# Kernel optimization log

Measured on AMD Instinct MI355X. Metric: run time of the kernel, lower is better.

Reference implementation:

```python
import jax, jax.numpy as jnp
import numpy as np

B, F_IN, C_NODES, M = 8, 32, 256, 64
C_OUT = 64
ORDER = 2
N_BASES = 3


def setup_inputs() -> dict:
    key = jax.random.key(0)
    ks = jax.random.split(key, 6)
    x = jax.random.normal(ks[0], (B, F_IN, C_NODES, M), dtype=jnp.float32)
    base0 = jax.random.uniform(ks[1], (B, M, C_NODES, C_NODES), dtype=jnp.float32) / C_NODES
    base1 = jax.random.uniform(ks[2], (B, M, C_NODES, C_NODES), dtype=jnp.float32) / C_NODES
    base2 = jax.random.uniform(ks[3], (B, M, C_NODES, C_NODES), dtype=jnp.float32) / C_NODES
    c_cat = (ORDER * N_BASES + 1) * F_IN  # 224
    W = jax.random.normal(ks[4], (C_OUT, c_cat), dtype=jnp.float32) * (1.0 / np.sqrt(c_cat))
    b = jnp.zeros((C_OUT,), dtype=jnp.float32)
    return {"x": x, "base0": base0, "base1": base1, "base2": base2, "W": W, "b": b}


def _nconv(x, A):
    # x: [B, F, n, M], A: [B, M, n, v] -> [B, F, v, M]
    return jnp.einsum('bfnm,bmnv->bfvm', x, A)


def reference(x, base0, base1, base2, W, b):
    out = [x]
    for A in (base0, base1, base2):
        x1 = _nconv(x, A)
        out.append(x1)
        for _ in range(2, ORDER + 1):
            x1 = _nconv(x1, A)
            out.append(x1)
    h = jnp.concatenate(out, axis=1)  # [B, 7F, C, M]
    # 1x1 conv == channel-mixing GEMM
    y = jnp.einsum('of,bfcm->bocm', W, h) + b[None, :, None, None]
    return y
```

## Files before the change

kernel.cpp:

```cpp
#include <hip/hip_runtime.h>

typedef __attribute__((ext_vector_type(8))) short short8;
typedef __attribute__((ext_vector_type(4))) float floatx4;
typedef unsigned short u16;
typedef unsigned int u32;

#define MFMA16(a,b,c) __builtin_amdgcn_mfma_f32_16x16x32_bf16((a),(b),(c),0,0,0)

#define GLD_LDS16(src, dst)                                                    \
  __builtin_amdgcn_global_load_lds(                                            \
      (const __attribute__((address_space(1))) u32*)(const u32*)(src),         \
      (__attribute__((address_space(3))) u32*)(u32*)(dst), 16, 0, 0)

#define WAITVM(N)                                                              \
  do {                                                                         \
    asm volatile("s_waitcnt vmcnt(" #N ")" ::: "memory");                      \
    __builtin_amdgcn_sched_barrier(0);                                         \
  } while (0)

#define WAITLGKM0() asm volatile("s_waitcnt lgkmcnt(0)" ::: "memory")

__device__ __forceinline__ void bar_lds() {
  WAITLGKM0();
  __builtin_amdgcn_s_barrier();
  asm volatile("" ::: "memory");
}

__device__ __forceinline__ u16 f2bf(float f) {
  u32 u = __builtin_bit_cast(u32, f);
  u += 0x7fffu + ((u >> 16) & 1u);
  return (u16)(u >> 16);
}
__device__ __forceinline__ u32 pk2(float a, float b) {
  return (u32)f2bf(a) | ((u32)f2bf(b) << 16);
}

__global__ __launch_bounds__(256) void tk_f2b(const float* __restrict__ in,
                                              u16* __restrict__ out,
                                              int NI, int NJ) {
  __shared__ float tile[64][65];
  const int tid = threadIdx.x;
  const long long base = (long long)blockIdx.z * NI * NJ;
  const int i0 = blockIdx.x * 64, j0 = blockIdx.y * 64;
#pragma unroll
  for (int p = 0; p < 4; ++p) {
    int i = p * 16 + (tid >> 4);
    int jl = (tid & 15) * 4;
    float4 v = *(const float4*)(in + base + (long long)(i0 + i) * NJ + j0 + jl);
    tile[i][jl + 0] = v.x; tile[i][jl + 1] = v.y;
    tile[i][jl + 2] = v.z; tile[i][jl + 3] = v.w;
  }
  __syncthreads();
#pragma unroll
  for (int p = 0; p < 4; ++p) {
    int j = p * 16 + (tid >> 4);
    int il = (tid & 15) * 4;
    float e0 = tile[il + 0][j], e1 = tile[il + 1][j];
    float e2 = tile[il + 2][j], e3 = tile[il + 3][j];
    uint2 o; o.x = pk2(e0, e1); o.y = pk2(e2, e3);
    *(uint2*)(out + base + (long long)(j0 + j) * NI + i0 + il) = o;
  }
}

__global__ __launch_bounds__(256) void tk_f2f(const float* __restrict__ in,
                                              float* __restrict__ out,
                                              int NI, int NJ) {
  __shared__ float tile[64][65];
  const int tid = threadIdx.x;
  const long long base = (long long)blockIdx.z * NI * NJ;
  const int i0 = blockIdx.x * 64, j0 = blockIdx.y * 64;
#pragma unroll
  for (int p = 0; p < 4; ++p) {
    int i = p * 16 + (tid >> 4);
    int jl = (tid & 15) * 4;
    float4 v = *(const float4*)(in + base + (long long)(i0 + i) * NJ + j0 + jl);
    tile[i][jl + 0] = v.x; tile[i][jl + 1] = v.y;
    tile[i][jl + 2] = v.z; tile[i][jl + 3] = v.w;
  }
  __syncthreads();
#pragma unroll
  for (int p = 0; p < 4; ++p) {
    int j = p * 16 + (tid >> 4);
    int il = (tid & 15) * 4;
    float4 o;
    o.x = tile[il + 0][j]; o.y = tile[il + 1][j];
    o.z = tile[il + 2][j]; o.w = tile[il + 3][j];
    *(float4*)(out + base + (long long)(j0 + j) * NI + i0 + il) = o;
  }
}

__global__ __launch_bounds__(256, 2) void gcn_main(
    const u16* __restrict__ xT, const float* __restrict__ A0,
    const float* __restrict__ A1, const float* __restrict__ A2,
    const float* __restrict__ Wm, const float* __restrict__ bias,
    float* __restrict__ yT) {
  __shared__ __align__(16) unsigned char smem[81920];
  unsigned char* ring   = smem;
  unsigned char* fragX1 = smem + 49152;
  unsigned char* fragH  = smem + 65536;

  const int tid  = threadIdx.x;
  const int w    = tid >> 6;
  const int lane = tid & 63;
  const int q    = lane >> 4;
  const int s    = lane & 15;
  const int wg   = blockIdx.x;

  const float* Acur  = A0 + (size_t)wg * 65536;
  const float* Anxt  = A1 + (size_t)wg * 65536;
  const float* Alast = A2 + (size_t)wg * 65536;

  const int lrow = (lane >> 4) << 8;
  const int lc0  = (w << 6) + ((lane & 15) << 2);
  const int lc1  = lc0 ^ 16;
  char* wring = (char*)ring + (w << 12);

  auto stage = [&](const float* Ap, int c, int slot) {
#pragma unroll
    for (int i = 0; i < 4; ++i) {
      const float* src = Ap + (c << 12) + (i << 10) + lrow + ((i & 2) ? lc1 : lc0);
      GLD_LDS16(src, wring + slot * 16384 + (i << 10));
    }
  };

  stage(Acur, 0, 0);
  stage(Acur, 1, 1);
  stage(Acur, 2, 2);

  short8 xa[2][8];
  const u16* xp = xT + (size_t)wg * 8192;
#pragma unroll
  for (int mr = 0; mr < 2; ++mr)
#pragma unroll
    for (int k = 0; k < 8; ++k)
      xa[mr][k] = *(const short8*)(xp + (16 * mr + s) * 256 + 32 * k + 8 * q);

#pragma unroll
  for (int mr = 0; mr < 2; ++mr)
#pragma unroll
    for (int kk = 0; kk < 8; ++kk) {
      if ((kk >> 1) != w) continue;
#pragma unroll
      for (int jj = 0; jj < 8; ++jj) {
        int c = 32 * kk + 8 * q + jj;
        int f = 16 * mr + s;
        int off = (((c >> 4) * 64 + (f >> 3) * 16 + (c & 15)) << 4) + 2 * (f & 7);
        *(u16*)(fragH + off) = (u16)xa[mr][kk][jj];
      }
    }

  floatx4 yacc[4][4];
#pragma unroll
  for (int mr = 0; mr < 4; ++mr)
#pragma unroll
    for (int t = 0; t < 4; ++t) yacc[mr][t] = (floatx4){0.f, 0.f, 0.f, 0.f};

  auto finalGemm = [&](int jblk) {
    short8 wf[4], hf[4];
#pragma unroll
    for (int mr = 0; mr < 4; ++mr) {
      const float* wp = Wm + (16 * mr + s) * 224 + 32 * jblk + 8 * q;
      float4 lo = *(const float4*)wp;
      float4 hi = *(const float4*)(wp + 4);
      union { uint4 u; short8 v; } r;
      r.u.x = pk2(lo.x, lo.y); r.u.y = pk2(lo.z, lo.w);
      r.u.z = pk2(hi.x, hi.y); r.u.w = pk2(hi.z, hi.w);
      wf[mr] = r.v;
    }
#pragma unroll
    for (int t = 0; t < 4; ++t)
      hf[t] = *(const short8*)(fragH + (((4 * w + t) * 64 + lane) << 4));
#pragma unroll
    for (int mr = 0; mr < 4; ++mr)
#pragma unroll
      for (int t = 0; t < 4; ++t)
        yacc[mr][t] = MFMA16(wf[mr], hf[t], yacc[mr][t]);
  };
  auto writeH = [&](const floatx4 (&acc)[2][4]) {
#pragma unroll
    for (int mr = 0; mr < 2; ++mr)
#pragma unroll
      for (int t = 0; t < 4; ++t)
#pragma unroll
        for (int r = 0; r < 4; ++r) {
          int F = 16 * mr + 4 * q + r;
          int off = (((4 * w + t) * 64 + (F >> 3) * 16 + s) << 4) + 2 * (F & 7);
          *(u16*)(fragH + off) = f2bf(acc[mr][t][r]);
        }
  };
  auto writeX1 = [&](const floatx4 (&acc)[2][4]) {
#pragma unroll
    for (int mr = 0; mr < 2; ++mr)
#pragma unroll
      for (int t = 0; t < 4; ++t) {
        int Cc = 64 * w + 16 * t + s;
        int kk = Cc >> 5, qq = (Cc >> 3) & 3, jj = Cc & 7;
#pragma unroll
        for (int r = 0; r < 4; ++r) {
          int off = (((mr * 8 + kk) * 64 + qq * 16 + 4 * q + r) << 4) + 2 * jj;
          *(u16*)(fragX1 + off) = f2bf(acc[mr][t][r]);
        }
      }
  };

  auto fetchB = [&](int sl0, int sl1, short8 (&bf)[4]) {
    const char* bse = (const char*)ring + ((q >= 2) ? sl1 : sl0) * 16384 +
                      (w << 12) + ((q & 1) << 11);
    const int pvx = (q & 1) << 4;
#pragma unroll
    for (int t = 0; t < 4; ++t) {
      const float* fp = (const float*)(bse + ((((t << 4) + s) ^ pvx) << 2));
      union { uint4 u; short8 v; } r;
      r.u.x = pk2(fp[0],   fp[64]);
      r.u.y = pk2(fp[128], fp[192]);
      r.u.z = pk2(fp[256], fp[320]);
      r.u.w = pk2(fp[384], fp[448]);
      bf[t] = r.v;
    }
  };

  finalGemm(0);

#pragma unroll 1
  for (int ib = 0; ib < 3; ++ib) {
    floatx4 h1[2][4];
#pragma unroll
    for (int mr = 0; mr < 2; ++mr)
#pragma unroll
      for (int t = 0; t < 4; ++t) h1[mr][t] = (floatx4){0.f, 0.f, 0.f, 0.f};
#pragma unroll
    for (int kk = 0; kk < 8; ++kk) {
      if (kk < 7) WAITVM(4); else WAITVM(0);
      short8 bf[4];
      fetchB((2 * kk) % 3, (2 * kk + 1) % 3, bf);
#pragma unroll
      for (int mr = 0; mr < 2; ++mr)
#pragma unroll
        for (int t = 0; t < 4; ++t)
          h1[mr][t] = MFMA16(xa[mr][kk], bf[t], h1[mr][t]);
      WAITLGKM0();
      if (kk < 6) {
        stage(Acur, 2 * kk + 3, (2 * kk + 3) % 3);
        stage(Acur, 2 * kk + 4, (2 * kk + 4) % 3);
      } else if (kk == 6) {
        stage(Acur, 15, 0);
      } else {
        stage(Acur, 0, 0); stage(Acur, 1, 1); stage(Acur, 2, 2);
      }
    }
    bar_lds();
    writeX1(h1);
    writeH(h1);
    bar_lds();
    finalGemm(1 + 2 * ib);

    floatx4 h2[2][4];
#pragma unroll
    for (int mr = 0; mr < 2; ++mr)
#pragma unroll
      for (int t = 0; t < 4; ++t) h2[mr][t] = (floatx4){0.f, 0.f, 0.f, 0.f};
#pragma unroll
    for (int kk = 0; kk < 8; ++kk) {
      if (kk < 7) WAITVM(4); else WAITVM(0);
      short8 bf[4];
      fetchB((2 * kk) % 3, (2 * kk + 1) % 3, bf);
      short8 a0 = *(const short8*)(fragX1 + ((kk * 64 + lane) << 4));
      short8 a1 = *(const short8*)(fragX1 + (((8 + kk) * 64 + lane) << 4));
#pragma unroll
      for (int t = 0; t < 4; ++t) {
        h2[0][t] = MFMA16(a0, bf[t], h2[0][t]);
        h2[1][t] = MFMA16(a1, bf[t], h2[1][t]);
      }
      WAITLGKM0();
      if (kk < 6) {
        stage(Acur, 2 * kk + 3, (2 * kk + 3) % 3);
        stage(Acur, 2 * kk + 4, (2 * kk + 4) % 3);
      } else if (kk == 6) {
        stage(Acur, 15, 0);
      } else if (ib < 2) {
        stage(Anxt, 0, 0); stage(Anxt, 1, 1); stage(Anxt, 2, 2);
      }
    }
    writeH(h2);
    finalGemm(2 + 2 * ib);

    Acur = Anxt; Anxt = Alast;
  }

  float* yp = yT + (size_t)wg * 16384;
#pragma unroll
  for (int mr = 0; mr < 4; ++mr) {
    float br[4];
#pragma unroll
    for (int r = 0; r < 4; ++r) br[r] = bias[16 * mr + 4 * q + r];
#pragma unroll
    for (int t = 0; t < 4; ++t) {
      int c = 64 * w + 16 * t + s;
#pragma unroll
      for (int r = 0; r < 4; ++r) {
        int o = 16 * mr + 4 * q + r;
        yp[o * 256 + c] = yacc[mr][t][r] + br[r];
      }
    }
  }
}

extern "C" void kernel_launch(void* const* d_in, const int* in_sizes, int n_in,
                              void* d_out, int out_size, void* d_ws, size_t ws_size,
                              hipStream_t stream) {
  const float* x    = (const float*)d_in[0];
  const float* b0   = (const float*)d_in[1];
  const float* b1   = (const float*)d_in[2];
  const float* b2   = (const float*)d_in[3];
  const float* Wm   = (const float*)d_in[4];
  const float* bias = (const float*)d_in[5];
  u16*   xT  = (u16*)d_ws;
  float* yTs = (float*)((char*)d_ws + 8388608);
  float* out = (float*)d_out;

  tk_f2b<<<dim3(128, 1, 8), 256, 0, stream>>>(x, xT, 8192, 64);
  gcn_main<<<dim3(512), 256, 0, stream>>>(xT, b0, b1, b2, Wm, bias, yTs);
  tk_f2f<<<dim3(1, 256, 8), 256, 0, stream>>>(yTs, out, 64, 16384);
}
```

Measured before the change: 481.6 us.

## Keep A fragments in registers across both hops and deepen the staging ring

```diff
diff --git a/kernel.cpp b/kernel.cpp
--- a/kernel.cpp
+++ b/kernel.cpp
@@ -89,15 +89,16 @@
   }
 }
 
-__global__ __launch_bounds__(256, 2) void gcn_main(
+__global__ __launch_bounds__(256, 1) void gcn_main(
     const u16* __restrict__ xT, const float* __restrict__ A0,
     const float* __restrict__ A1, const float* __restrict__ A2,
     const float* __restrict__ Wm, const float* __restrict__ bias,
     float* __restrict__ yT) {
-  __shared__ __align__(16) unsigned char smem[81920];
+  __shared__ __align__(16) unsigned char smem[126976];
   unsigned char* ring   = smem;
-  unsigned char* fragX1 = smem + 49152;
-  unsigned char* fragH  = smem + 65536;
+  unsigned char* fragX1 = smem + 65536;
+  unsigned char* fragH  = smem + 81920;
+  unsigned char* wLds   = smem + 98304;
 
   const int tid  = threadIdx.x;
   const int w    = tid >> 6;
@@ -126,6 +127,20 @@
   stage(Acur, 0, 0);
   stage(Acur, 1, 1);
   stage(Acur, 2, 2);
+  stage(Acur, 3, 3);
+
+#pragma unroll 2
+  for (int jb = w; jb < 7; jb += 4)
+#pragma unroll
+    for (int mr = 0; mr < 4; ++mr) {
+      const float* wp = Wm + (16 * mr + s) * 224 + 32 * jb + 8 * q;
+      float4 lo = *(const float4*)wp;
+      float4 hi = *(const float4*)(wp + 4);
+      uint4 r;
+      r.x = pk2(lo.x, lo.y); r.y = pk2(lo.z, lo.w);
+      r.z = pk2(hi.x, hi.y); r.w = pk2(hi.z, hi.w);
+      *(uint4*)(wLds + (((jb * 4 + mr) * 64 + lane) << 4)) = r;
+    }
 
   short8 xa[2][8];
   const u16* xp = xT + (size_t)wg * 8192;
@@ -158,15 +173,8 @@
   auto finalGemm = [&](int jblk) {
     short8 wf[4], hf[4];
 #pragma unroll
-    for (int mr = 0; mr < 4; ++mr) {
-      const float* wp = Wm + (16 * mr + s) * 224 + 32 * jblk + 8 * q;
-      float4 lo = *(const float4*)wp;
-      float4 hi = *(const float4*)(wp + 4);
-      union { uint4 u; short8 v; } r;
-      r.u.x = pk2(lo.x, lo.y); r.u.y = pk2(lo.z, lo.w);
-      r.u.z = pk2(hi.x, hi.y); r.u.w = pk2(hi.z, hi.w);
-      wf[mr] = r.v;
-    }
+    for (int mr = 0; mr < 4; ++mr)
+      wf[mr] = *(const short8*)(wLds + (((jblk * 4 + mr) * 64 + lane) << 4));
 #pragma unroll
     for (int t = 0; t < 4; ++t)
       hf[t] = *(const short8*)(fragH + (((4 * w + t) * 64 + lane) << 4));
@@ -219,7 +227,10 @@
     }
   };
 
+  bar_lds();
   finalGemm(0);
+
+  short8 afrag[8][4];
 
 #pragma unroll 1
   for (int ib = 0; ib < 3; ++ib) {
@@ -230,23 +241,28 @@
       for (int t = 0; t < 4; ++t) h1[mr][t] = (floatx4){0.f, 0.f, 0.f, 0.f};
 #pragma unroll
     for (int kk = 0; kk < 8; ++kk) {
-      if (kk < 7) WAITVM(4); else WAITVM(0);
-      short8 bf[4];
-      fetchB((2 * kk) % 3, (2 * kk + 1) % 3, bf);
+      if (kk == 7) {
+        if (ib == 2) WAITVM(0); else WAITVM(8);
+      } else {
+        WAITVM(8);
+      }
+      fetchB((2 * kk) & 3, (2 * kk + 1) & 3, afrag[kk]);
+      WAITLGKM0();
+      {
+        const int cn = 2 * kk + 4;
+        if (cn < 16) {
+          stage(Acur, cn, cn & 3);
+          stage(Acur, cn + 1, (cn + 1) & 3);
+        } else if (ib < 2) {
+          stage(Anxt, cn - 16, (cn - 16) & 3);
+          stage(Anxt, cn - 15, (cn - 15) & 3);
+        }
+      }
 #pragma unroll
       for (int mr = 0; mr < 2; ++mr)
 #pragma unroll
         for (int t = 0; t < 4; ++t)
-          h1[mr][t] = MFMA16(xa[mr][kk], bf[t], h1[mr][t]);
-      WAITLGKM0();
-      if (kk < 6) {
-        stage(Acur, 2 * kk + 3, (2 * kk + 3) % 3);
-        stage(Acur, 2 * kk + 4, (2 * kk + 4) % 3);
-      } else if (kk == 6) {
-        stage(Acur, 15, 0);
-      } else {
-        stage(Acur, 0, 0); stage(Acur, 1, 1); stage(Acur, 2, 2);
-      }
+          h1[mr][t] = MFMA16(xa[mr][kk], afrag[kk][t], h1[mr][t]);
     }
     bar_lds();
     writeX1(h1);
@@ -261,24 +277,12 @@
       for (int t = 0; t < 4; ++t) h2[mr][t] = (floatx4){0.f, 0.f, 0.f, 0.f};
 #pragma unroll
     for (int kk = 0; kk < 8; ++kk) {
-      if (kk < 7) WAITVM(4); else WAITVM(0);
-      short8 bf[4];
-      fetchB((2 * kk) % 3, (2 * kk + 1) % 3, bf);
       short8 a0 = *(const short8*)(fragX1 + ((kk * 64 + lane) << 4));
       short8 a1 = *(const short8*)(fragX1 + (((8 + kk) * 64 + lane) << 4));
 #pragma unroll
       for (int t = 0; t < 4; ++t) {
-        h2[0][t] = MFMA16(a0, bf[t], h2[0][t]);
-        h2[1][t] = MFMA16(a1, bf[t], h2[1][t]);
-      }
-      WAITLGKM0();
-      if (kk < 6) {
-        stage(Acur, 2 * kk + 3, (2 * kk + 3) % 3);
-        stage(Acur, 2 * kk + 4, (2 * kk + 4) % 3);
-      } else if (kk == 6) {
-        stage(Acur, 15, 0);
-      } else if (ib < 2) {
-        stage(Anxt, 0, 0); stage(Anxt, 1, 1); stage(Anxt, 2, 2);
+        h2[0][t] = MFMA16(a0, afrag[kk][t], h2[0][t]);
+        h2[1][t] = MFMA16(a1, afrag[kk][t], h2[1][t]);
       }
     }
     writeH(h2);
```

Result: faster. 392.2 us (-18.6%).
